# Optimization experiments

Measured on AMD Instinct MI355X. Metric: run time of the kernel, lower is better.

Reference implementation:

```python
import jax, jax.numpy as jnp
import numpy as np

DIM = 2048
NUM_HEADS = 16
NUM_KV_HEADS = 4
HEAD_DIM = DIM // NUM_HEADS  # 128
ROPE_BASE = 10000.0
CLIP = 31.0
BLOCK = 128


def fake_quant(w):
    """Blockwise int-ish fake quantization, steady QAT state (ratio=1, clip=31, no noise)."""
    out_f, in_f = w.shape
    pad = (-in_f) % BLOCK
    wp = jnp.pad(w, ((0, 0), (0, pad)))
    wb = wp.reshape(-1, BLOCK)
    # scale computed under no_grad in torch -> stop_gradient
    bmax = jnp.max(jnp.abs(wb), axis=1)
    s = jnp.maximum(bmax / CLIP, 1e-12).astype(jnp.float16)
    s = jnp.maximum(s, jnp.finfo(jnp.float16).tiny).astype(jnp.float32)
    s = jax.lax.stop_gradient(s)[:, None]
    ws = wb / s
    q = ws - jax.lax.stop_gradient(ws) + jax.lax.stop_gradient(
        jnp.round(jnp.clip(ws, -(CLIP + 1.0), CLIP)))  # STE
    qw = (q * s).reshape(out_f, in_f + pad)
    return qw[:, :in_f] if pad > 0 else qw


def rms_norm(x):
    eps = jnp.finfo(x.dtype).eps
    return x * jax.lax.rsqrt(jnp.mean(x * x, axis=-1, keepdims=True) + eps)


def rope_tables(seqlen, dtype):
    inv_freq = 1.0 / (ROPE_BASE ** (jnp.arange(0, HEAD_DIM, 2, dtype=jnp.float32) / HEAD_DIM))
    freqs = jnp.outer(jnp.arange(seqlen, dtype=jnp.float32), inv_freq)  # [S, hd/2]
    return jnp.cos(freqs).astype(dtype), jnp.sin(freqs).astype(dtype)


def apply_rotary(x, cos, sin):
    # x: [B,H,S,hd]; cos/sin: [S,hd/2]
    half = x.shape[-1] // 2
    x1, x2 = x[..., :half], x[..., half:]
    return jnp.concatenate((x1 * cos + x2 * sin, -x1 * sin + x2 * cos), axis=-1)


def setup_inputs() -> dict:
    key = jax.random.key(0)
    ks = jax.random.split(key, 6)
    kv_dim = NUM_KV_HEADS * HEAD_DIM
    std = DIM ** -0.5
    return {
        "x": jax.random.normal(ks[0], (2, 2048, DIM), dtype=jnp.float32),
        "Wq": jax.random.normal(ks[1], (DIM, DIM), dtype=jnp.float32) * std,
        "Wk": jax.random.normal(ks[2], (kv_dim, DIM), dtype=jnp.float32) * std,
        "Wv": jax.random.normal(ks[3], (kv_dim, DIM), dtype=jnp.float32) * std,
        "Wproj": jax.random.normal(ks[4], (DIM, DIM), dtype=jnp.float32) * std,
        "q_gain": jnp.full((NUM_HEADS,), 1.0, dtype=jnp.float32),
    }


def reference(x, Wq, Wk, Wv, Wproj, q_gain):
    B, S, D = x.shape
    H, KV, hd = NUM_HEADS, NUM_KV_HEADS, HEAD_DIM
    q = (x @ fake_quant(Wq).T).reshape(B, S, H, hd).transpose(0, 2, 1, 3)   # [B,H,S,hd]
    k = (x @ fake_quant(Wk).T).reshape(B, S, KV, hd).transpose(0, 2, 1, 3)  # [B,KV,S,hd]
    v = (x @ fake_quant(Wv).T).reshape(B, S, KV, hd).transpose(0, 2, 1, 3)
    q = rms_norm(q)
    k = rms_norm(k)
    cos, sin = rope_tables(S, q.dtype)
    q = apply_rotary(q, cos, sin)
    k = apply_rotary(k, cos, sin)
    q = q * q_gain[None, :, None, None]
    # GQA: expand kv heads
    rep = H // KV
    k = jnp.repeat(k, rep, axis=1)  # [B,H,S,hd]
    v = jnp.repeat(v, rep, axis=1)
    scale = 1.0 / jnp.sqrt(jnp.asarray(hd, dtype=q.dtype))
    scores = jnp.einsum("bhqd,bhkd->bhqk", q, k) * scale
    causal = jnp.tril(jnp.ones((S, S), dtype=bool))
    scores = jnp.where(causal, scores, jnp.asarray(-jnp.inf, dtype=scores.dtype))
    attn = jax.nn.softmax(scores, axis=-1)
    y = jnp.einsum("bhqk,bhkd->bhqd", attn, v)  # [B,H,S,hd]
    y = y.transpose(0, 2, 1, 3).reshape(B, S, D)
    return y @ fake_quant(Wproj).T
```

## Files before the change

kernel.cpp:

```cpp
#include <hip/hip_runtime.h>
#include <hip/hip_bf16.h>
#include <hip/hip_fp16.h>

#define SEQ    2048
#define DMODEL 2048
#define NH     16
#define NKV    4
#define HD     128
#define NTOT   3072
#define MROWS  4096

typedef __attribute__((ext_vector_type(4))) float f32x4;
typedef __attribute__((ext_vector_type(8))) __bf16 bf16x8;
typedef __attribute__((ext_vector_type(8))) unsigned short u16x8;
typedef __attribute__((ext_vector_type(4))) unsigned short u16x4;

__device__ __forceinline__ void async_copy16(const void* g, void* l) {
  __builtin_amdgcn_global_load_lds(
      (const __attribute__((address_space(1))) void*)g,
      (__attribute__((address_space(3))) void*)l, 16, 0, 0);
}

__device__ __forceinline__ unsigned short fto16(float f) {
  __hip_bfloat16 h = __float2bfloat16(f);
  return *(unsigned short*)&h;
}

__device__ __forceinline__ float b2f(unsigned short u) {
  unsigned int t = (unsigned int)u << 16;
  float f;
  __builtin_memcpy(&f, &t, 4);
  return f;
}

__global__ __launch_bounds__(256) void fq_kernel(const float* __restrict__ Wq,
                                                 const float* __restrict__ Wk,
                                                 const float* __restrict__ Wv,
                                                 const float* __restrict__ Wp,
                                                 unsigned short* __restrict__ Wcat,
                                                 unsigned short* __restrict__ Wpq) {
  int g = blockIdx.x * 4 + (threadIdx.x >> 6);
  int lane = threadIdx.x & 63;
  const float* W;
  unsigned short* out;
  int blk;
  if (g < 32768)      { W = Wq; out = Wcat;                          blk = g; }
  else if (g < 40960) { W = Wk; out = Wcat + (size_t)2048 * 2048;    blk = g - 32768; }
  else if (g < 49152) { W = Wv; out = Wcat + (size_t)2560 * 2048;    blk = g - 40960; }
  else                { W = Wp; out = Wpq;                           blk = g - 49152; }
  const float* p = W + (size_t)blk * 128 + lane * 2;
  float w0 = p[0], w1 = p[1];
  float m = fmaxf(fabsf(w0), fabsf(w1));
#pragma unroll
  for (int o = 32; o; o >>= 1) m = fmaxf(m, __shfl_xor(m, o));
  float s = fmaxf(m / 31.0f, 1e-12f);
  s = __half2float(__float2half(s));
  s = fmaxf(s, 6.103515625e-05f);
  float q0 = rintf(fminf(fmaxf(w0 / s, -32.0f), 31.0f)) * s;
  float q1 = rintf(fminf(fmaxf(w1 / s, -32.0f), 31.0f)) * s;
  unsigned short* o16 = out + (size_t)blk * 128 + lane * 2;
  o16[0] = fto16(q0);
  o16[1] = fto16(q1);
}

__global__ __launch_bounds__(256) void conv_kernel(const float* __restrict__ in,
                                                   unsigned short* __restrict__ out,
                                                   int n) {
  int i = (blockIdx.x * blockDim.x + threadIdx.x) * 4;
  if (i >= n) return;
  float4 v = *(const float4*)(in + i);
  ushort4 o;
  o.x = fto16(v.x); o.y = fto16(v.y); o.z = fto16(v.z); o.w = fto16(v.w);
  *(ushort4*)(out + i) = o;
}

#define BM 128
#define BN 128
#define BK 32
template <typename OT>
__global__ __launch_bounds__(256) void gemm_bt(const unsigned short* __restrict__ A,
                                               const unsigned short* __restrict__ Bm,
                                               OT* __restrict__ C,
                                               int M, int N, int K) {
  __shared__ unsigned short As[BM * BK];
  __shared__ unsigned short Bs[BN * BK];
  const int tid = threadIdx.x;
  const int wave = tid >> 6, lane = tid & 63;
  const int quad = lane >> 4, l16 = lane & 15;
  const int m0 = blockIdx.x * BM, n0 = blockIdx.y * BN;
  const int wm = (wave >> 1) * 64, wn = (wave & 1) * 64;
  const int sr = lane >> 2, sc = (lane & 3) * 8;

  const unsigned short* Ag = A + (size_t)m0 * K;
  const unsigned short* Bg = Bm + (size_t)n0 * K;

  f32x4 acc[4][4];
#pragma unroll
  for (int i = 0; i < 4; i++)
#pragma unroll
    for (int j = 0; j < 4; j++) acc[i][j] = f32x4{0.f, 0.f, 0.f, 0.f};

  const int seg0 = wave * 2, seg1 = wave * 2 + 1;
  unsigned short* lA0 = &As[seg0 * 16 * BK];
  unsigned short* lA1 = &As[seg1 * 16 * BK];
  unsigned short* lB0 = &Bs[seg0 * 16 * BK];
  unsigned short* lB1 = &Bs[seg1 * 16 * BK];
  const unsigned short* gA0 = Ag + (size_t)(seg0 * 16 + sr) * K + sc;
  const unsigned short* gA1 = Ag + (size_t)(seg1 * 16 + sr) * K + sc;
  const unsigned short* gB0 = Bg + (size_t)(seg0 * 16 + sr) * K + sc;
  const unsigned short* gB1 = Bg + (size_t)(seg1 * 16 + sr) * K + sc;

  for (int k0 = 0; k0 < K; k0 += BK) {
    __syncthreads();
    async_copy16(gA0 + k0, lA0);
    async_copy16(gA1 + k0, lA1);
    async_copy16(gB0 + k0, lB0);
    async_copy16(gB1 + k0, lB1);
    __syncthreads();
    bf16x8 af[4], bf[4];
#pragma unroll
    for (int t = 0; t < 4; t++)
      af[t] = *(const bf16x8*)&As[(wm + t * 16 + l16) * BK + quad * 8];
#pragma unroll
    for (int t = 0; t < 4; t++)
      bf[t] = *(const bf16x8*)&Bs[(wn + t * 16 + l16) * BK + quad * 8];
#pragma unroll
    for (int i = 0; i < 4; i++)
#pragma unroll
      for (int j = 0; j < 4; j++)
        acc[i][j] = __builtin_amdgcn_mfma_f32_16x16x32_bf16(af[i], bf[j], acc[i][j], 0, 0, 0);
  }
#pragma unroll
  for (int i = 0; i < 4; i++) {
    int row_base = m0 + wm + i * 16 + quad * 4;
#pragma unroll
    for (int j = 0; j < 4; j++) {
      int col = n0 + wn + j * 16 + l16;
#pragma unroll
      for (int r = 0; r < 4; r++) {
        if constexpr (sizeof(OT) == 2)
          C[(size_t)(row_base + r) * N + col] = fto16(acc[i][j][r]);
        else
          C[(size_t)(row_base + r) * N + col] = acc[i][j][r];
      }
    }
  }
}

#define QSCALE 0.12751791437524245f
__global__ __launch_bounds__(256) void normrope_kernel(const unsigned short* __restrict__ qkvb,
                                                       const float* __restrict__ qgain,
                                                       unsigned short* __restrict__ qbuf,
                                                       unsigned short* __restrict__ kbuf) {
  const int i = blockIdx.x;
  const int bz = i >> 11, tok = i & 2047;
  const int wave = threadIdx.x >> 6, lane = threadIdx.x & 63;
  const unsigned short* row = qkvb + (size_t)i * NTOT;

  double invf = pow(10000.0, -(double)(2 * lane) / 128.0);
  float freq = (float)((double)tok * invf);
  float cs = cosf(freq), sn = sinf(freq);

  for (int slot = wave; slot < 20; slot += 4) {
    if (slot < 16) {
      int hh = slot;
      const unsigned short* src = row + hh * HD;
      float x1 = b2f(src[lane]), x2 = b2f(src[lane + 64]);
      float ss = x1 * x1 + x2 * x2;
#pragma unroll
      for (int o = 32; o; o >>= 1) ss += __shfl_xor(ss, o);
      float rn = rsqrtf(ss * (1.0f / 128.0f) + 1.1920929e-07f);
      float n1 = x1 * rn, n2 = x2 * rn;
      float g = qgain[hh] * QSCALE;
      unsigned short* dst = qbuf + ((size_t)(bz * NH + hh) * SEQ + tok) * HD;
      dst[lane]      = fto16((n1 * cs + n2 * sn) * g);
      dst[lane + 64] = fto16((-n1 * sn + n2 * cs) * g);
    } else {
      int hh = slot - 16;
      const unsigned short* src = row + DMODEL + hh * HD;
      float x1 = b2f(src[lane]), x2 = b2f(src[lane + 64]);
      float ss = x1 * x1 + x2 * x2;
#pragma unroll
      for (int o = 32; o; o >>= 1) ss += __shfl_xor(ss, o);
      float rn = rsqrtf(ss * (1.0f / 128.0f) + 1.1920929e-07f);
      float n1 = x1 * rn, n2 = x2 * rn;
      unsigned short* dst = kbuf + ((size_t)(bz * NKV + hh) * SEQ + tok) * HD;
      dst[lane]      = fto16(n1 * cs + n2 * sn);
      dst[lane + 64] = fto16(-n1 * sn + n2 * cs);
    }
  }
}

__global__ __launch_bounds__(256) void vtrans_kernel(const unsigned short* __restrict__ qkvb,
                                                     unsigned short* __restrict__ vtb) {
  __shared__ unsigned short T[64 * 72];
  const int s0 = blockIdx.x * 64;
  const int d0 = blockIdx.y * 64;
  const int bz = blockIdx.z >> 2, h = blockIdx.z & 3;
  const int tid = threadIdx.x;
#pragma unroll
  for (int i = 0; i < 2; ++i) {
    int c = i * 256 + tid;
    int s = c >> 3, ch = c & 7;
    const unsigned short* src =
        qkvb + (size_t)(bz * SEQ + s0 + s) * NTOT + DMODEL + 512 + h * HD + d0 + ch * 8;
    *(u16x8*)&T[s * 72 + ch * 8] = *(const u16x8*)src;
  }
  __syncthreads();
  unsigned short* outg = vtb + (size_t)(bz * NKV + h) * HD * SEQ;
#pragma unroll
  for (int i = 0; i < 2; ++i) {
    int c = i * 256 + tid;
    int d = c >> 3, sc = c & 7;
    u16x8 v;
#pragma unroll
    for (int j = 0; j < 8; ++j) v[j] = T[(sc * 8 + j) * 72 + d];
    *(u16x8*)(outg + (size_t)(d0 + d) * SEQ + s0 + sc * 8) = v;
  }
}

__global__ __launch_bounds__(256, 2) void attn_kernel(const unsigned short* __restrict__ qb,
                                                      const unsigned short* __restrict__ kb,
                                                      const unsigned short* __restrict__ vtb,
                                                      unsigned short* __restrict__ yb) {
  __shared__ unsigned short Ks[64 * 128];
  __shared__ unsigned short Vt[128 * 64];
  __shared__ unsigned short Ps[4][32 * 64];

  const int bx = blockIdx.x;
  const int h = blockIdx.y;
  const int bz = blockIdx.z;
  const int qt = bz ? bx : (15 - bx);
  const int tid = threadIdx.x;
  const int wave = tid >> 6, lane = tid & 63;
  const int quad = lane >> 4, l16 = lane & 15;
  const int q0 = qt * 128;
  const int base0 = q0 + wave * 32;
  const int base1 = base0 + 16;
  const int kdiag0 = base0 >> 6, kdiag1 = base1 >> 6;

  const unsigned short* qg = qb + (size_t)(bz * NH + h) * SEQ * HD;
  const unsigned short* kg = kb + (size_t)(bz * NKV + (h >> 2)) * SEQ * HD;
  const unsigned short* vg = vtb + (size_t)(bz * NKV + (h >> 2)) * HD * SEQ;
  unsigned short* psw = &Ps[wave][0];

  bf16x8 qf[2][4];
#pragma unroll
  for (int sg = 0; sg < 2; ++sg)
#pragma unroll
    for (int ds = 0; ds < 4; ++ds)
      qf[sg][ds] = *(const bf16x8*)(qg + (size_t)(base0 + sg * 16 + l16) * HD + ds * 32 + quad * 8);

  f32x4 oacc[2][8];
#pragma unroll
  for (int sg = 0; sg < 2; ++sg)
#pragma unroll
    for (int j = 0; j < 8; ++j) oacc[sg][j] = f32x4{0.f, 0.f, 0.f, 0.f};
  float m_i[2] = {-__builtin_inff(), -__builtin_inff()};
  float l_i[2] = {0.f, 0.f};

  const int krw = tid >> 4, kgr = tid & 15;
  const int vdw = tid >> 3, vgr = tid & 7;

  const int nkt = 2 * qt + 2;

  u16x8 pk[4], pv[4];
#pragma unroll
  for (int i = 0; i < 4; ++i)
    pk[i] = *(const u16x8*)(kg + (size_t)(i * 16 + krw) * HD + kgr * 8);
#pragma unroll
  for (int i = 0; i < 4; ++i)
    pv[i] = *(const u16x8*)(vg + (size_t)(i * 32 + vdw) * SEQ + vgr * 8);

  for (int kt = 0; kt < nkt; ++kt) {
#pragma unroll
    for (int i = 0; i < 4; ++i) {
      int row = i * 16 + krw;
      *(u16x8*)&Ks[row * 128 + ((kgr ^ (row & 15)) << 3)] = pk[i];
    }
#pragma unroll
    for (int i = 0; i < 4; ++i) {
      int d = i * 32 + vdw;
      *(u16x8*)&Vt[d * 64 + ((vgr ^ (d & 7)) << 3)] = pv[i];
    }
    __syncthreads();

    if (kt + 1 < nkt) {
#pragma unroll
      for (int i = 0; i < 4; ++i)
        pk[i] = *(const u16x8*)(kg + (size_t)((kt + 1) * 64 + i * 16 + krw) * HD + kgr * 8);
#pragma unroll
      for (int i = 0; i < 4; ++i)
        pv[i] = *(const u16x8*)(vg + (size_t)(i * 32 + vdw) * SEQ + (kt + 1) * 64 + vgr * 8);
    }

    const bool act0 = (kt <= kdiag0);
    if (kt <= kdiag1) {
      f32x4 st[2][4];
#pragma unroll
      for (int sg = 0; sg < 2; ++sg)
#pragma unroll
        for (int mt = 0; mt < 4; ++mt) st[sg][mt] = f32x4{0.f, 0.f, 0.f, 0.f};
#pragma unroll
      for (int mt = 0; mt < 4; ++mt)
#pragma unroll
        for (int ds = 0; ds < 4; ++ds) {
          bf16x8 kf = *(const bf16x8*)&Ks[(mt * 16 + l16) * 128 + ((((ds << 2) + quad) ^ l16) << 3)];
          if (act0)
            st[0][mt] = __builtin_amdgcn_mfma_f32_16x16x32_bf16(kf, qf[0][ds], st[0][mt], 0, 0, 0);
          st[1][mt] = __builtin_amdgcn_mfma_f32_16x16x32_bf16(kf, qf[1][ds], st[1][mt], 0, 0, 0);
        }

#pragma unroll
      for (int sg = 0; sg < 2; ++sg) {
        if (sg == 0 && !act0) continue;
        const int base = sg ? base1 : base0;
        const int qrow = base + l16;
        float p[4][4];
        float mx = -__builtin_inff();
        if (kt == (sg ? kdiag1 : kdiag0)) {
#pragma unroll
          for (int mt = 0; mt < 4; ++mt)
#pragma unroll
            for (int r = 0; r < 4; ++r) {
              int kp = kt * 64 + mt * 16 + quad * 4 + r;
              float v = (kp <= qrow) ? st[sg][mt][r] : -__builtin_inff();
              p[mt][r] = v;
              mx = fmaxf(mx, v);
            }
        } else {
#pragma unroll
          for (int mt = 0; mt < 4; ++mt)
#pragma unroll
            for (int r = 0; r < 4; ++r) {
              p[mt][r] = st[sg][mt][r];
              mx = fmaxf(mx, st[sg][mt][r]);
            }
        }
        mx = fmaxf(mx, __shfl_xor(mx, 16));
        mx = fmaxf(mx, __shfl_xor(mx, 32));
        float mnew = fmaxf(m_i[sg], mx);
        float rs = 0.f;
#pragma unroll
        for (int mt = 0; mt < 4; ++mt)
#pragma unroll
          for (int r = 0; r < 4; ++r) {
            float e = exp2f(p[mt][r] - mnew);
            p[mt][r] = e;
            rs += e;
          }
        rs += __shfl_xor(rs, 16);
        rs += __shfl_xor(rs, 32);
        if (__any(mnew > m_i[sg])) {
          float a = exp2f(m_i[sg] - mnew);
#pragma unroll
          for (int j = 0; j < 8; ++j) oacc[sg][j] *= a;
          l_i[sg] = l_i[sg] * a + rs;
        } else {
          l_i[sg] += rs;
        }
        m_i[sg] = mnew;

        const int rq = sg * 16 + l16;
#pragma unroll
        for (int mt = 0; mt < 4; ++mt) {
          u16x4 w;
#pragma unroll
          for (int r = 0; r < 4; ++r) w[r] = fto16(p[mt][r]);
          int g = mt * 2 + (quad >> 1);
          *(u16x4*)&psw[rq * 64 + ((g ^ (l16 & 7)) << 3) + (quad & 1) * 4] = w;
        }
      }

      __asm__ volatile("s_waitcnt lgkmcnt(0)" ::: "memory");

#pragma unroll
      for (int c = 0; c < 2; ++c) {
        bf16x8 pf0, pf1;
        if (act0)
          pf0 = *(const bf16x8*)&psw[l16 * 64 + ((((c << 2) + quad) ^ (l16 & 7)) << 3)];
        pf1 = *(const bf16x8*)&psw[(16 + l16) * 64 + ((((c << 2) + quad) ^ (l16 & 7)) << 3)];
#pragma unroll
        for (int mt = 0; mt < 8; ++mt) {
          bf16x8 vf = *(const bf16x8*)&Vt[(mt * 16 + l16) * 64 + ((((c << 2) + quad) ^ (l16 & 7)) << 3)];
          if (act0)
            oacc[0][mt] = __builtin_amdgcn_mfma_f32_16x16x32_bf16(vf, pf0, oacc[0][mt], 0, 0, 0);
          oacc[1][mt] = __builtin_amdgcn_mfma_f32_16x16x32_bf16(vf, pf1, oacc[1][mt], 0, 0, 0);
        }
      }
    }
    __syncthreads();
  }

#pragma unroll
  for (int sg = 0; sg < 2; ++sg) {
    float il = 1.0f / l_i[sg];
    int qrow = base0 + sg * 16 + l16;
#pragma unroll
    for (int mt = 0; mt < 8; ++mt) {
      u16x4 o;
#pragma unroll
      for (int r = 0; r < 4; ++r) o[r] = fto16(oacc[sg][mt][r] * il);
      *(u16x4*)&yb[(size_t)(bz * SEQ + qrow) * DMODEL + h * HD + mt * 16 + quad * 4] = o;
    }
  }
}

extern "C" void kernel_launch(void* const* d_in, const int* in_sizes, int n_in,
                              void* d_out, int out_size, void* d_ws, size_t ws_size,
                              hipStream_t stream) {
  (void)in_sizes; (void)n_in; (void)out_size; (void)ws_size;
  const float* x  = (const float*)d_in[0];
  const float* Wq = (const float*)d_in[1];
  const float* Wk = (const float*)d_in[2];
  const float* Wv = (const float*)d_in[3];
  const float* Wp = (const float*)d_in[4];
  const float* qg = (const float*)d_in[5];
  float* out = (float*)d_out;
  char* ws = (char*)d_ws;

  unsigned short* xb   = (unsigned short*)(ws + 0);
  unsigned short* Wcat = (unsigned short*)(ws + 16777216);
  unsigned short* Wpq  = (unsigned short*)(ws + 29360128);
  unsigned short* qkvb = (unsigned short*)(ws + 37748736);
  unsigned short* qbuf = (unsigned short*)(ws + 62914560);
  unsigned short* kbuf = (unsigned short*)(ws + 79691776);
  unsigned short* vtb  = (unsigned short*)(ws + 83886080);
  unsigned short* yb   = xb;

  fq_kernel<<<81920 / 4, 256, 0, stream>>>(Wq, Wk, Wv, Wp, Wcat, Wpq);
  conv_kernel<<<8388608 / 1024, 256, 0, stream>>>(x, xb, 8388608);
  gemm_bt<unsigned short><<<dim3(32, 24), 256, 0, stream>>>(xb, Wcat, qkvb, MROWS, NTOT, DMODEL);
  normrope_kernel<<<MROWS, 256, 0, stream>>>(qkvb, qg, qbuf, kbuf);
  vtrans_kernel<<<dim3(32, 2, 8), 256, 0, stream>>>(qkvb, vtb);
  attn_kernel<<<dim3(16, NH, 2), 256, 0, stream>>>(qbuf, kbuf, vtb, yb);
  gemm_bt<float><<<dim3(32, 16), 256, 0, stream>>>(yb, Wpq, out, MROWS, DMODEL, DMODEL);
}
```

Baseline: 336.7 us.

## Split attention block into 8 waves with 16 query rows each

The attention kernel now runs 512 threads per block. Each of the 8 waves handles 16 query rows instead of two 16-row groups, and the per-wave P staging buffers shrink to match. This halves per-wave register state (accumulators, Q fragments) so more waves can be resident to hide latency, and it spreads the cooperative K/V tile loads over more threads. The trade-off is that each wave now reads the K and V fragments from LDS for only 16 rows, so LDS traffic per MFMA doubles, and more waves are contending at each barrier.

```diff
diff --git a/kernel.cpp b/kernel.cpp
--- a/kernel.cpp
+++ b/kernel.cpp
@@ -219,13 +219,13 @@
   }
 }
 
-__global__ __launch_bounds__(256, 2) void attn_kernel(const unsigned short* __restrict__ qb,
+__global__ __launch_bounds__(512, 4) void attn_kernel(const unsigned short* __restrict__ qb,
                                                       const unsigned short* __restrict__ kb,
                                                       const unsigned short* __restrict__ vtb,
                                                       unsigned short* __restrict__ yb) {
   __shared__ unsigned short Ks[64 * 128];
   __shared__ unsigned short Vt[128 * 64];
-  __shared__ unsigned short Ps[4][32 * 64];
+  __shared__ unsigned short Ps[8][16 * 64];
 
   const int bx = blockIdx.x;
   const int h = blockIdx.y;
@@ -235,172 +235,150 @@
   const int wave = tid >> 6, lane = tid & 63;
   const int quad = lane >> 4, l16 = lane & 15;
   const int q0 = qt * 128;
-  const int base0 = q0 + wave * 32;
-  const int base1 = base0 + 16;
-  const int kdiag0 = base0 >> 6, kdiag1 = base1 >> 6;
+  const int base = q0 + wave * 16;
+  const int kdiag = base >> 6;
 
   const unsigned short* qg = qb + (size_t)(bz * NH + h) * SEQ * HD;
   const unsigned short* kg = kb + (size_t)(bz * NKV + (h >> 2)) * SEQ * HD;
   const unsigned short* vg = vtb + (size_t)(bz * NKV + (h >> 2)) * HD * SEQ;
   unsigned short* psw = &Ps[wave][0];
 
-  bf16x8 qf[2][4];
-#pragma unroll
-  for (int sg = 0; sg < 2; ++sg)
-#pragma unroll
-    for (int ds = 0; ds < 4; ++ds)
-      qf[sg][ds] = *(const bf16x8*)(qg + (size_t)(base0 + sg * 16 + l16) * HD + ds * 32 + quad * 8);
-
-  f32x4 oacc[2][8];
-#pragma unroll
-  for (int sg = 0; sg < 2; ++sg)
-#pragma unroll
-    for (int j = 0; j < 8; ++j) oacc[sg][j] = f32x4{0.f, 0.f, 0.f, 0.f};
-  float m_i[2] = {-__builtin_inff(), -__builtin_inff()};
-  float l_i[2] = {0.f, 0.f};
+  bf16x8 qf[4];
+#pragma unroll
+  for (int ds = 0; ds < 4; ++ds)
+    qf[ds] = *(const bf16x8*)(qg + (size_t)(base + l16) * HD + ds * 32 + quad * 8);
+
+  f32x4 oacc[8];
+#pragma unroll
+  for (int j = 0; j < 8; ++j) oacc[j] = f32x4{0.f, 0.f, 0.f, 0.f};
+  float m_i = -__builtin_inff();
+  float l_i = 0.f;
 
   const int krw = tid >> 4, kgr = tid & 15;
   const int vdw = tid >> 3, vgr = tid & 7;
 
   const int nkt = 2 * qt + 2;
 
-  u16x8 pk[4], pv[4];
-#pragma unroll
-  for (int i = 0; i < 4; ++i)
-    pk[i] = *(const u16x8*)(kg + (size_t)(i * 16 + krw) * HD + kgr * 8);
-#pragma unroll
-  for (int i = 0; i < 4; ++i)
-    pv[i] = *(const u16x8*)(vg + (size_t)(i * 32 + vdw) * SEQ + vgr * 8);
+  u16x8 pk[2], pv[2];
+#pragma unroll
+  for (int i = 0; i < 2; ++i)
+    pk[i] = *(const u16x8*)(kg + (size_t)(i * 32 + krw) * HD + kgr * 8);
+#pragma unroll
+  for (int i = 0; i < 2; ++i)
+    pv[i] = *(const u16x8*)(vg + (size_t)(i * 64 + vdw) * SEQ + vgr * 8);
 
   for (int kt = 0; kt < nkt; ++kt) {
 #pragma unroll
-    for (int i = 0; i < 4; ++i) {
-      int row = i * 16 + krw;
+    for (int i = 0; i < 2; ++i) {
+      int row = i * 32 + krw;
       *(u16x8*)&Ks[row * 128 + ((kgr ^ (row & 15)) << 3)] = pk[i];
     }
 #pragma unroll
-    for (int i = 0; i < 4; ++i) {
-      int d = i * 32 + vdw;
+    for (int i = 0; i < 2; ++i) {
+      int d = i * 64 + vdw;
       *(u16x8*)&Vt[d * 64 + ((vgr ^ (d & 7)) << 3)] = pv[i];
     }
     __syncthreads();
 
     if (kt + 1 < nkt) {
 #pragma unroll
-      for (int i = 0; i < 4; ++i)
-        pk[i] = *(const u16x8*)(kg + (size_t)((kt + 1) * 64 + i * 16 + krw) * HD + kgr * 8);
-#pragma unroll
-      for (int i = 0; i < 4; ++i)
-        pv[i] = *(const u16x8*)(vg + (size_t)(i * 32 + vdw) * SEQ + (kt + 1) * 64 + vgr * 8);
-    }
-
-    const bool act0 = (kt <= kdiag0);
-    if (kt <= kdiag1) {
-      f32x4 st[2][4];
-#pragma unroll
-      for (int sg = 0; sg < 2; ++sg)
-#pragma unroll
-        for (int mt = 0; mt < 4; ++mt) st[sg][mt] = f32x4{0.f, 0.f, 0.f, 0.f};
+      for (int i = 0; i < 2; ++i)
+        pk[i] = *(const u16x8*)(kg + (size_t)((kt + 1) * 64 + i * 32 + krw) * HD + kgr * 8);
+#pragma unroll
+      for (int i = 0; i < 2; ++i)
+        pv[i] = *(const u16x8*)(vg + (size_t)(i * 64 + vdw) * SEQ + (kt + 1) * 64 + vgr * 8);
+    }
+
+    if (kt <= kdiag) {
+      f32x4 st[4];
+#pragma unroll
+      for (int mt = 0; mt < 4; ++mt) st[mt] = f32x4{0.f, 0.f, 0.f, 0.f};
 #pragma unroll
       for (int mt = 0; mt < 4; ++mt)
 #pragma unroll
         for (int ds = 0; ds < 4; ++ds) {
           bf16x8 kf = *(const bf16x8*)&Ks[(mt * 16 + l16) * 128 + ((((ds << 2) + quad) ^ l16) << 3)];
-          if (act0)
-            st[0][mt] = __builtin_amdgcn_mfma_f32_16x16x32_bf16(kf, qf[0][ds], st[0][mt], 0, 0, 0);
-          st[1][mt] = __builtin_amdgcn_mfma_f32_16x16x32_bf16(kf, qf[1][ds], st[1][mt], 0, 0, 0);
+          st[mt] = __builtin_amdgcn_mfma_f32_16x16x32_bf16(kf, qf[ds], st[mt], 0, 0, 0);
         }
 
-#pragma unroll
-      for (int sg = 0; sg < 2; ++sg) {
-        if (sg == 0 && !act0) continue;
-        const int base = sg ? base1 : base0;
-        const int qrow = base + l16;
-        float p[4][4];
-        float mx = -__builtin_inff();
-        if (kt == (sg ? kdiag1 : kdiag0)) {
-#pragma unroll
-          for (int mt = 0; mt < 4; ++mt)
-#pragma unroll
-            for (int r = 0; r < 4; ++r) {
-              int kp = kt * 64 + mt * 16 + quad * 4 + r;
-              float v = (kp <= qrow) ? st[sg][mt][r] : -__builtin_inff();
-              p[mt][r] = v;
-              mx = fmaxf(mx, v);
-            }
-        } else {
-#pragma unroll
-          for (int mt = 0; mt < 4; ++mt)
-#pragma unroll
-            for (int r = 0; r < 4; ++r) {
-              p[mt][r] = st[sg][mt][r];
-              mx = fmaxf(mx, st[sg][mt][r]);
-            }
+      const int qrow = base + l16;
+      float p[4][4];
+      float mx = -__builtin_inff();
+      if (kt == kdiag) {
+#pragma unroll
+        for (int mt = 0; mt < 4; ++mt)
+#pragma unroll
+          for (int r = 0; r < 4; ++r) {
+            int kp = kt * 64 + mt * 16 + quad * 4 + r;
+            float v = (kp <= qrow) ? st[mt][r] : -__builtin_inff();
+            p[mt][r] = v;
+            mx = fmaxf(mx, v);
+          }
+      } else {
+#pragma unroll
+        for (int mt = 0; mt < 4; ++mt)
+#pragma unroll
+          for (int r = 0; r < 4; ++r) {
+            p[mt][r] = st[mt][r];
+            mx = fmaxf(mx, st[mt][r]);
+          }
+      }
+      mx = fmaxf(mx, __shfl_xor(mx, 16));
+      mx = fmaxf(mx, __shfl_xor(mx, 32));
+      float mnew = fmaxf(m_i, mx);
+      float rs = 0.f;
+#pragma unroll
+      for (int mt = 0; mt < 4; ++mt)
+#pragma unroll
+        for (int r = 0; r < 4; ++r) {
+          float e = exp2f(p[mt][r] - mnew);
+          p[mt][r] = e;
+          rs += e;
         }
-        mx = fmaxf(mx, __shfl_xor(mx, 16));
-        mx = fmaxf(mx, __shfl_xor(mx, 32));
-        float mnew = fmaxf(m_i[sg], mx);
-        float rs = 0.f;
-#pragma unroll
-        for (int mt = 0; mt < 4; ++mt)
-#pragma unroll
-          for (int r = 0; r < 4; ++r) {
-            float e = exp2f(p[mt][r] - mnew);
-            p[mt][r] = e;
-            rs += e;
-          }
-        rs += __shfl_xor(rs, 16);
-        rs += __shfl_xor(rs, 32);
-        if (__any(mnew > m_i[sg])) {
-          float a = exp2f(m_i[sg] - mnew);
-#pragma unroll
-          for (int j = 0; j < 8; ++j) oacc[sg][j] *= a;
-          l_i[sg] = l_i[sg] * a + rs;
-        } else {
-          l_i[sg] += rs;
-        }
-        m_i[sg] = mnew;
-
-        const int rq = sg * 16 + l16;
-#pragma unroll
-        for (int mt = 0; mt < 4; ++mt) {
-          u16x4 w;
-#pragma unroll
-          for (int r = 0; r < 4; ++r) w[r] = fto16(p[mt][r]);
-          int g = mt * 2 + (quad >> 1);
-          *(u16x4*)&psw[rq * 64 + ((g ^ (l16 & 7)) << 3) + (quad & 1) * 4] = w;
+      rs += __shfl_xor(rs, 16);
+      rs += __shfl_xor(rs, 32);
+      if (__any(mnew > m_i)) {
+        float a = exp2f(m_i - mnew);
+#pragma unroll
+        for (int j = 0; j < 8; ++j) oacc[j] *= a;
+        l_i = l_i * a + rs;
+      } else {
+        l_i += rs;
+      }
+      m_i = mnew;
+
+#pragma unroll
+      for (int mt = 0; mt < 4; ++mt) {
+        u16x4 w;
+#pragma unroll
+        for (int r = 0; r < 4; ++r) w[r] = fto16(p[mt][r]);
+        int g = mt * 2 + (quad >> 1);
+        *(u16x4*)&psw[l16 * 64 + ((g ^ (l16 & 7)) << 3) + (quad & 1) * 4] = w;
+      }
+
+      __asm__ volatile("s_waitcnt lgkmcnt(0)" ::: "memory");
+
+#pragma unroll
+      for (int c = 0; c < 2; ++c) {
+        bf16x8 pf = *(const bf16x8*)&psw[l16 * 64 + ((((c << 2) + quad) ^ (l16 & 7)) << 3)];
+#pragma unroll
+        for (int mt = 0; mt < 8; ++mt) {
+          bf16x8 vf = *(const bf16x8*)&Vt[(mt * 16 + l16) * 64 + ((((c << 2) + quad) ^ (l16 & 7)) << 3)];
+          oacc[mt] = __builtin_amdgcn_mfma_f32_16x16x32_bf16(vf, pf, oacc[mt], 0, 0, 0);
         }
       }
-
-      __asm__ volatile("s_waitcnt lgkmcnt(0)" ::: "memory");
-
-#pragma unroll
-      for (int c = 0; c < 2; ++c) {
-        bf16x8 pf0, pf1;
-        if (act0)
-          pf0 = *(const bf16x8*)&psw[l16 * 64 + ((((c << 2) + quad) ^ (l16 & 7)) << 3)];
-        pf1 = *(const bf16x8*)&psw[(16 + l16) * 64 + ((((c << 2) + quad) ^ (l16 & 7)) << 3)];
-#pragma unroll
-        for (int mt = 0; mt < 8; ++mt) {
-          bf16x8 vf = *(const bf16x8*)&Vt[(mt * 16 + l16) * 64 + ((((c << 2) + quad) ^ (l16 & 7)) << 3)];
-          if (act0)
-            oacc[0][mt] = __builtin_amdgcn_mfma_f32_16x16x32_bf16(vf, pf0, oacc[0][mt], 0, 0, 0);
-          oacc[1][mt] = __builtin_amdgcn_mfma_f32_16x16x32_bf16(vf, pf1, oacc[1][mt], 0, 0, 0);
-        }
-      }
     }
     __syncthreads();
   }
 
-#pragma unroll
-  for (int sg = 0; sg < 2; ++sg) {
-    float il = 1.0f / l_i[sg];
-    int qrow = base0 + sg * 16 + l16;
+  {
+    float il = 1.0f / l_i;
+    int qrow = base + l16;
 #pragma unroll
     for (int mt = 0; mt < 8; ++mt) {
       u16x4 o;
 #pragma unroll
-      for (int r = 0; r < 4; ++r) o[r] = fto16(oacc[sg][mt][r] * il);
+      for (int r = 0; r < 4; ++r) o[r] = fto16(oacc[mt][r] * il);
       *(u16x4*)&yb[(size_t)(bz * SEQ + qrow) * DMODEL + h * HD + mt * 16 + quad * 4] = o;
     }
   }
@@ -433,6 +411,6 @@
   gemm_bt<unsigned short><<<dim3(32, 24), 256, 0, stream>>>(xb, Wcat, qkvb, MROWS, NTOT, DMODEL);
   normrope_kernel<<<MROWS, 256, 0, stream>>>(qkvb, qg, qbuf, kbuf);
   vtrans_kernel<<<dim3(32, 2, 8), 256, 0, stream>>>(qkvb, vtb);
-  attn_kernel<<<dim3(16, NH, 2), 256, 0, stream>>>(qbuf, kbuf, vtb, yb);
+  attn_kernel<<<dim3(16, NH, 2), 512, 0, stream>>>(qbuf, kbuf, vtb, yb);
   gemm_bt<float><<<dim3(32, 16), 256, 0, stream>>>(yb, Wpq, out, MROWS, DMODEL, DMODEL);
 }
```

Measured after the change: 331.3 us. About the same (-1.6%).
